# Kernel tuning notes

Measured on AMD Instinct MI355X. Metric: run time of the kernel, lower is better.

## Reference

```python
import jax, jax.numpy as jnp
import numpy as np
import math


def _strided_value_mask(L, S, dtype):
    # mask_line[L + d] == 0 when |d| is a power-of-two stride in {2,4,...,<=L};
    # value_mask[i, j] = mask_line[L - i + j], i.e. zero where |j - i| is such a stride.
    diff = jnp.abs(jnp.arange(L)[:, None] - jnp.arange(S)[None, :])  # [L, S]
    vm = jnp.ones((L, S), dtype=dtype)
    stride = 2
    while stride <= L:
        vm = vm * (diff != stride).astype(dtype)
        stride *= 2
    return vm


def setup_inputs() -> dict:
    key = jax.random.key(0)
    k1, k2, k3 = jax.random.split(key, 3)
    B, L, H, E = 4, 2048, 8, 64
    D = 64
    return {
        "queries": jax.random.normal(k1, (B, L, H, E), dtype=jnp.float32),
        "keys": jax.random.normal(k2, (B, L, H, E), dtype=jnp.float32),
        "values": jax.random.normal(k3, (B, L, H, D), dtype=jnp.float32),
    }


def reference(queries, keys, values):
    B, L, H, E = queries.shape
    S = keys.shape[1]
    scale = 1.0 / math.sqrt(E)

    # raw scores [B, H, L, S]
    scores = jnp.einsum("blhe,bshe->bhls", queries, keys)
    # multiplicative strided mask (zeroes scores at power-of-two offsets)
    vm = _strided_value_mask(L, S, scores.dtype)  # [L, S]
    scores = scores * vm
    # causal mask: upper triangle -> -inf (mask_flag=True, attn_mask=None path)
    causal = jnp.triu(jnp.ones((L, S), dtype=bool), k=1)
    scores = jnp.where(causal, -jnp.inf, scores)

    # dropout p=0.0 (eval) -> identity
    A = jax.nn.softmax(scale * scores, axis=-1)
    V = jnp.einsum("bhls,bshd->blhd", A, values)
    return V
```

## Files before the change

### kernel.cpp

```cpp
#include <hip/hip_runtime.h>
#include <hip/hip_bf16.h>
#include <stdint.h>

typedef __attribute__((ext_vector_type(8))) short short8;
typedef __attribute__((ext_vector_type(16))) float f32x16;

namespace {
constexpr int NB = 4, NL = 2048, NH = 8, NE = 64, ND = 64;
constexpr float KS = 0.125f * 1.44269504f;
constexpr int RECSZ32 = 2080;
constexpr int NUNIT   = 160;
constexpr int NCHUNK = 40;
constexpr int RECSZ  = 8320;
constexpr int KSTEP  = 64 * NH * NE;
}

__device__ const unsigned char ORD[160] = {
  63,127,191,255,
  48,112,176, 49,113,177, 50,114,178, 51,115,179, 52,116,180,
  53,117,181, 54,118,182, 55,119,183, 56,120,184, 57,121,185,
  58,122,186, 59,123,187, 60,124,188, 61,125,189, 62,126,190,
  47,111,175,
  32,96, 33,97, 34,98, 35,99, 36,100, 37,101, 38,102, 39,103,
  40,104, 41,105, 42,106, 43,107, 44,108, 45,109, 46,110,
  31,95,
  15,16,17,18,19,20,21,22,23,24,25,26,27,28,29,30,
  14,94,174,254, 13,93,173,253, 12,92,172,252, 11,91,171,251,
  10,90,170,250,  9,89,169,249,  8,88,168,248,  7,87,167,247,
   6,86,166,246,  5,85,165,245,  4,84,164,244,  3,83,163,243,
   2,82,162,242,  1,81,161,241,  0,80,160,240};

__device__ const unsigned char TG[40] = {
  3,7,7,10,11,11,11,14,14,15,15,15,15,
  6,6,9,9,10,10,12,12,13,13,13,13,14,14,
  2,5,5,8,8,8,9,12,12,
  4,4,1,0};
__device__ const unsigned char TT0[40] = {
  0,0,16,0,0,16,32,0,16,0,16,32,48,
  0,14,0,14,16,30,0,14,0,14,28,42,32,46,
  0,0,12,0,12,24,28,28,40,
  0,10,0,0};
__device__ const unsigned char TT1[40] = {
  16,16,32,16,16,32,48,16,32,16,32,48,64,
  14,28,14,28,30,44,14,28,14,28,42,56,46,60,
  12,12,24,12,24,36,40,40,52,
  10,20,8,4};
__device__ const unsigned char TREC[40] = {
  3,10,11,18,21,22,23,32,33,36,37,38,39,
  8,9,15,16,19,20,24,25,28,29,30,31,34,35,
  2,6,7,12,13,14,17,26,27,
  4,5,1,0};
__device__ const unsigned char CUMD[16] = {0,1,2,3,4,6,8,10,12,15,18,21,24,28,32,36};
__device__ const unsigned char NCHD[16] = {1,1,1,1,2,2,2,2,3,3,3,3,4,4,4,4};

__device__ __forceinline__ ushort bfb(float x) {
  __hip_bfloat16 b(x);
  return __builtin_bit_cast(ushort, b);
}
__device__ __forceinline__ uint32_t pkbf(float lo, float hi) {
  return (uint32_t)bfb(lo) | ((uint32_t)bfb(hi) << 16);
}


__global__ __launch_bounds__(256)
void convfrag(const float* __restrict__ Kg, const float* __restrict__ Vg,
              char* __restrict__ kimg, char* __restrict__ vimg)
{
  const int id = blockIdx.x;
  const int kr = id & 31, bh = id >> 5;
  const int b = bh >> 3, h = bh & 7;
  const int tid = threadIdx.x;

  __shared__ __align__(16) char  kt[64 * 128];
  __shared__ __align__(16) float vt[64 * 64];

  const int key = tid >> 2;
  const int e0  = (tid & 3) * 16;
  {
    const float* kp = Kg + (((size_t)b * NL + kr * 64 + key) * NH + h) * NE + e0;
    float4 a = *(const float4*)kp,       c = *(const float4*)(kp + 4);
    float4 d2 = *(const float4*)(kp + 8), f = *(const float4*)(kp + 12);
    uint4 wA = { pkbf(a.x,a.y), pkbf(a.z,a.w), pkbf(c.x,c.y), pkbf(c.z,c.w) };
    uint4 wB = { pkbf(d2.x,d2.y), pkbf(d2.z,d2.w), pkbf(f.x,f.y), pkbf(f.z,f.w) };
    const int sw = (key & 7) << 4;
    *(uint4*)(kt + key * 128 + ((2 * e0)      ^ sw)) = wA;
    *(uint4*)(kt + key * 128 + ((2 * e0 + 16) ^ sw)) = wB;
  }
  {
    const float* vp = Vg + (((size_t)b * NL + kr * 64 + key) * NH + h) * ND + e0;
    float* dst = vt + key * 64 + e0;
    *(float4*)(dst)      = *(const float4*)(vp);
    *(float4*)(dst + 4)  = *(const float4*)(vp + 4);
    *(float4*)(dst + 8)  = *(const float4*)(vp + 8);
    *(float4*)(dst + 12) = *(const float4*)(vp + 12);
  }
  __syncthreads();

  char* kob = kimg + (size_t)bh * 262144 + (size_t)kr * 2 * 4096;
  char* vob = vimg + (size_t)bh * 262144 + (size_t)kr * 2 * 4096;
  #pragma unroll
  for (int it = 0; it < 2; ++it) {
    int lin = it * 256 + tid;
    int fi = lin >> 6, l = lin & 63;
    int tt = fi >> 2, st = fi & 3;
    int ky = tt * 32 + (l & 31);
    int e  = st * 16 + (l >> 5) * 8;
    uint4 w = *(const uint4*)(kt + ky * 128 + ((2 * e) ^ ((ky & 7) << 4)));
    *(uint4*)(kob + tt * 4096 + st * 1024 + l * 16) = w;
  }
  #pragma unroll
  for (int it = 0; it < 2; ++it) {
    int lin = it * 256 + tid;
    int fi = lin >> 6, l = lin & 63;
    int tt = fi >> 2, f = fi & 3;
    int d  = (f >> 1) * 32 + (l & 31);
    int k0 = tt * 32 + (f & 1) * 16 + (l >> 5) * 8;
    const float* c0 = vt + k0 * 64 + d;
    uint4 w = { pkbf(c0[0],   c0[64]),  pkbf(c0[128], c0[192]),
                pkbf(c0[256], c0[320]), pkbf(c0[384], c0[448]) };
    *(uint4*)(vob + tt * 4096 + f * 1024 + l * 16) = w;
  }
}

__global__ __launch_bounds__(128)
void sattn_frag(const float* __restrict__ Qg, const char* __restrict__ kimg,
                const char* __restrict__ vimg, float* __restrict__ W)
{
  const int id   = blockIdx.x;
  const int bh   = id & 31;
  const int pair = id >> 5;
  const int b = bh >> 3, h = bh & 7;

  const int tid  = threadIdx.x;
  const int wave = tid >> 6;
  const int lane = tid & 63;
  const int ln31 = lane & 31;
  const int hi   = lane >> 5;

  const int e   = ORD[pair * 2 + wave];
  const int s   = e & 63, k = e >> 6;
  const int t0u = k * 16;
  const int t1u = (t0u + 16 < s + 1) ? t0u + 16 : s + 1;
  const int G   = s >> 4;
  const int rix = 8 * G * (G + 1) + (s & 15) * (G + 1) + k;
  float* rec = W + ((size_t)bh * NUNIT + rix) * RECSZ32;

  const int q0w = s * 32;
  const int qi  = q0w + ln31;
  const char* kb_img = kimg + (size_t)bh * 262144 + lane * 16;
  const char* vb_img = vimg + (size_t)bh * 262144 + lane * 16;

  short8 qf[4];
  {
    const float* qp = Qg + (((size_t)b * NL + qi) * NH + h) * NE;
    #pragma unroll
    for (int st = 0; st < 4; ++st) {
      const float* qpe = qp + st * 16 + hi * 8;
      union { short8 v; uint32_t u[4]; } f;
      #pragma unroll
      for (int j = 0; j < 4; ++j)
        f.u[j] = pkbf(qpe[2 * j] * KS, qpe[2 * j + 1] * KS);
      qf[st] = f.v;
    }
  }
  short8 onesv;
  {
    union { short8 v; uint32_t u[4]; } o;
    #pragma unroll
    for (int j = 0; j < 4; ++j) o.u[j] = 0x3F803F80u;
    onesv = o.v;
  }

  f32x16 acc0, acc1, accl;
  #pragma unroll
  for (int i = 0; i < 16; ++i) { acc0[i] = 0.f; acc1[i] = 0.f; accl[i] = 0.f; }

  for (int t = t0u; t < t1u; ++t) {
    const char* kp = kb_img + (size_t)t * 4096;
    const char* vp = vb_img + (size_t)t * 4096;
    short8 a00 = *(const short8*)(vp);
    short8 a01 = *(const short8*)(vp + 1024);
    short8 a10 = *(const short8*)(vp + 2048);
    short8 a11 = *(const short8*)(vp + 3072);
    short8 kf0 = *(const short8*)(kp);
    short8 kf1 = *(const short8*)(kp + 1024);
    short8 kf2 = *(const short8*)(kp + 2048);
    short8 kf3 = *(const short8*)(kp + 3072);

    f32x16 sv;
    #pragma unroll
    for (int i = 0; i < 16; ++i) sv[i] = 0.f;
    sv = __builtin_amdgcn_mfma_f32_32x32x16_bf16(kf0, qf[0], sv, 0, 0, 0);
    sv = __builtin_amdgcn_mfma_f32_32x32x16_bf16(kf1, qf[1], sv, 0, 0, 0);
    sv = __builtin_amdgcn_mfma_f32_32x32x16_bf16(kf2, qf[2], sv, 0, 0, 0);
    sv = __builtin_amdgcn_mfma_f32_32x32x16_bf16(kf3, qf[3], sv, 0, 0, 0);

    const int kv0 = t * 32;
    const int delta = q0w - kv0;
    const int qrelh = (qi - kv0) - 4 * hi;
    if (t == s) {
      #pragma unroll
      for (int r = 0; r < 16; ++r) {
        const int cr = (r & 3) + 8 * (r >> 2);
        int diff = qrelh - cr;
        float lg = sv[r];
        bool p2 = (diff > 1) & ((diff & (diff - 1)) == 0);
        lg = p2 ? 0.f : lg;
        lg = (diff < 0) ? -__builtin_inff() : lg;
        sv[r] = exp2f(lg);
      }
    } else {
      int pmax = 1 << (31 - __clz(delta + 31));
      if (pmax >= delta - 31) {
        #pragma unroll
        for (int r = 0; r < 16; ++r) {
          const int cr = (r & 3) + 8 * (r >> 2);
          int diff = qrelh - cr;
          bool p2 = (diff > 1) & ((diff & (diff - 1)) == 0);
          sv[r] = exp2f(p2 ? 0.f : sv[r]);
        }
      } else {
        #pragma unroll
        for (int r = 0; r < 16; ++r) sv[r] = exp2f(sv[r]);
      }
    }

    uint32_t w0 = pkbf(sv[0],  sv[1]),  w1 = pkbf(sv[2],  sv[3]);
    uint32_t w2 = pkbf(sv[4],  sv[5]),  w3 = pkbf(sv[6],  sv[7]);
    uint32_t w4 = pkbf(sv[8],  sv[9]),  w5 = pkbf(sv[10], sv[11]);
    uint32_t w6 = pkbf(sv[12], sv[13]), w7 = pkbf(sv[14], sv[15]);
    uint32_t y0 = __shfl_xor(hi ? w0 : w2, 32);
    uint32_t y1 = __shfl_xor(hi ? w1 : w3, 32);
    uint32_t y2 = __shfl_xor(hi ? w4 : w6, 32);
    uint32_t y3 = __shfl_xor(hi ? w5 : w7, 32);
    union { short8 v; uint32_t u[4]; } f0, f1;
    if (hi == 0) {
      f0.u[0] = w0; f0.u[1] = w1; f0.u[2] = y0; f0.u[3] = y1;
      f1.u[0] = w4; f1.u[1] = w5; f1.u[2] = y2; f1.u[3] = y3;
    } else {
      f0.u[0] = y0; f0.u[1] = y1; f0.u[2] = w2; f0.u[3] = w3;
      f1.u[0] = y2; f1.u[1] = y3; f1.u[2] = w6; f1.u[3] = w7;
    }

    acc0 = __builtin_amdgcn_mfma_f32_32x32x16_bf16(a00, f0.v, acc0, 0, 0, 0);
    acc0 = __builtin_amdgcn_mfma_f32_32x32x16_bf16(a01, f1.v, acc0, 0, 0, 0);
    acc1 = __builtin_amdgcn_mfma_f32_32x32x16_bf16(a10, f0.v, acc1, 0, 0, 0);
    acc1 = __builtin_amdgcn_mfma_f32_32x32x16_bf16(a11, f1.v, acc1, 0, 0, 0);
    accl = __builtin_amdgcn_mfma_f32_32x32x16_bf16(onesv, f0.v, accl, 0, 0, 0);
    accl = __builtin_amdgcn_mfma_f32_32x32x16_bf16(onesv, f1.v, accl, 0, 0, 0);
  }

  #pragma unroll
  for (int r = 0; r < 16; ++r) {
    int d = (r & 3) + 8 * (r >> 2) + 4 * hi;
    rec[d * 32 + ln31]        = acc0[r];
    rec[(32 + d) * 32 + ln31] = acc1[r];
  }
  if (hi == 0) rec[2048 + ln31] = accl[0];
}

__global__ __launch_bounds__(256)
void sattn_combine32(const float* __restrict__ W, float* __restrict__ Og)
{
  const int id = blockIdx.x;
  const int s  = id & 63, bh = id >> 6;
  const int b = bh >> 3, h = bh & 7;
  const int tid = threadIdx.x;

  const int G = s >> 4, i = s & 15;
  const int cum = 8 * G * (G + 1) + i * (G + 1);
  const int nc  = G + 1;
  const float* rec0 = W + ((size_t)bh * NUNIT + cum) * RECSZ32;

  __shared__ float sd[64][33];
  __shared__ float Lq[32];

  {
    int d = tid >> 2, q4 = (tid & 3) * 8;
    float4 a0 = {0,0,0,0}, a1 = {0,0,0,0};
    for (int c = 0; c < nc; ++c) {
      const float* rp = rec0 + (size_t)c * RECSZ32 + d * 32 + q4;
      float4 v0 = *(const float4*)rp, v1 = *(const float4*)(rp + 4);
      a0.x += v0.x; a0.y += v0.y; a0.z += v0.z; a0.w += v0.w;
      a1.x += v1.x; a1.y += v1.y; a1.z += v1.z; a1.w += v1.w;
    }
    sd[d][q4+0] = a0.x; sd[d][q4+1] = a0.y; sd[d][q4+2] = a0.z; sd[d][q4+3] = a0.w;
    sd[d][q4+4] = a1.x; sd[d][q4+5] = a1.y; sd[d][q4+6] = a1.z; sd[d][q4+7] = a1.w;
  }
  if (tid < 32) {
    float a = 0.f;
    for (int c = 0; c < nc; ++c) a += rec0[(size_t)c * RECSZ32 + 2048 + tid];
    Lq[tid] = 1.0f / a;
  }
  __syncthreads();
  {
    int q = tid >> 3, d8 = (tid & 7) * 8;
    float l = Lq[q];
    float4 o0 = { sd[d8+0][q]*l, sd[d8+1][q]*l, sd[d8+2][q]*l, sd[d8+3][q]*l };
    float4 o1 = { sd[d8+4][q]*l, sd[d8+5][q]*l, sd[d8+6][q]*l, sd[d8+7][q]*l };
    float* op = Og + (((size_t)b * NL + s * 32 + q) * NH + h) * ND + d8;
    *(float4*)op = o0; *(float4*)(op + 4) = o1;
  }
}

#define LD(RR) do {                                                         \
    const float* kp_ = kpp + (size_t)(RR) * KSTEP;                          \
    const float* vp_ = vpp + (size_t)(RR) * KSTEP;                          \
    kx0 = *(const float4*)(kp_);      kx1 = *(const float4*)(kp_ + 4);      \
    kx2 = *(const float4*)(kp_ + 8);  kx3 = *(const float4*)(kp_ + 12);     \
    vx0 = *(const float4*)(vp_);               vx1 = *(const float4*)(vp_ + NH*ND); \
    vx2 = *(const float4*)(vp_ + 2*NH*ND);     vx3 = *(const float4*)(vp_ + 3*NH*ND); \
  } while (0)

#define STG(KB, VB) do {                                                    \
    uint4 kwA = { pkbf(kx0.x,kx0.y), pkbf(kx0.z,kx0.w),                     \
                  pkbf(kx1.x,kx1.y), pkbf(kx1.z,kx1.w) };                   \
    uint4 kwB = { pkbf(kx2.x,kx2.y), pkbf(kx2.z,kx2.w),                     \
                  pkbf(kx3.x,kx3.y), pkbf(kx3.z,kx3.w) };                   \
    *(uint4*)((KB) + krow*128 + ( kcol2        ^ kswz)) = kwA;              \
    *(uint4*)((KB) + krow*128 + ((kcol2 + 16)  ^ kswz)) = kwB;              \
    _Pragma("unroll")                                                       \
    for (int j_ = 0; j_ < 4; ++j_) {                                        \
      int d_ = vd0 + j_;                                                    \
      char* vr_ = (VB) + d_*128;                                            \
      int vs_ = (d_ & 7) << 4;                                              \
      *(uint32_t*)(vr_ + ((vk0*2    ) ^ vs_)) = pkbf(vx0[j_], vx1[j_]);     \
      *(uint32_t*)(vr_ + ((vk0*2 + 4) ^ vs_)) = pkbf(vx2[j_], vx3[j_]);     \
    }                                                                       \
  } while (0)

#define COMPUTE(TT, SUB, KB, VB) do {                                       \
    const int kv0_ = (TT) * 32;                                             \
    f32x16 s;                                                               \
    _Pragma("unroll")                                                       \
    for (int i_ = 0; i_ < 16; ++i_) s[i_] = 0.f;                            \
    { const char* kb_ = (const char*)(KB) + ((SUB)*32 + ln31) * 128;        \
      _Pragma("unroll")                                                     \
      for (int st_ = 0; st_ < 4; ++st_) {                                   \
        short8 kf_ = *(const short8*)(kb_ + ((st_*32 + hi*16) ^ rsw));      \
        s = __builtin_amdgcn_mfma_f32_32x32x16_bf16(kf_, qf[st_], s, 0,0,0);\
      } }                                                                   \
    const int delta_ = q0w - kv0_;                                          \
    const int qrelh_ = (qi - kv0_) - 4 * hi;                                \
    if ((TT) == tw) {                                                       \
      _Pragma("unroll")                                                     \
      for (int r_ = 0; r_ < 16; ++r_) {                                     \
        const int cr_ = (r_ & 3) + 8 * (r_ >> 2);                           \
        int diff_ = qrelh_ - cr_;                                           \
        float lg_ = s[r_];                                                  \
        bool p2_ = (diff_ > 1) & ((diff_ & (diff_ - 1)) == 0);              \
        lg_ = p2_ ? 0.f : lg_;                                              \
        lg_ = (diff_ < 0) ? -__builtin_inff() : lg_;                        \
        s[r_] = exp2f(lg_);                                                 \
      }                                                                     \
    } else {                                                                \
      int pmax_ = 1 << (31 - __clz(delta_ + 31));                           \
      if (pmax_ >= delta_ - 31) {                                           \
        _Pragma("unroll")                                                   \
        for (int r_ = 0; r_ < 16; ++r_) {                                   \
          const int cr_ = (r_ & 3) + 8 * (r_ >> 2);                         \
          int diff_ = qrelh_ - cr_;                                         \
          bool p2_ = (diff_ > 1) & ((diff_ & (diff_ - 1)) == 0);            \
          s[r_] = exp2f(p2_ ? 0.f : s[r_]);                                 \
        }                                                                   \
      } else {                                                              \
        _Pragma("unroll")                                                   \
        for (int r_ = 0; r_ < 16; ++r_) s[r_] = exp2f(s[r_]);               \
      }                                                                     \
    }                                                                       \
    uint32_t w0_ = pkbf(s[0],  s[1]),  w1_ = pkbf(s[2],  s[3]);             \
    uint32_t w2_ = pkbf(s[4],  s[5]),  w3_ = pkbf(s[6],  s[7]);             \
    uint32_t w4_ = pkbf(s[8],  s[9]),  w5_ = pkbf(s[10], s[11]);            \
    uint32_t w6_ = pkbf(s[12], s[13]), w7_ = pkbf(s[14], s[15]);            \
    uint32_t y0_ = __shfl_xor(hi ? w0_ : w2_, 32);                          \
    uint32_t y1_ = __shfl_xor(hi ? w1_ : w3_, 32);                          \
    uint32_t y2_ = __shfl_xor(hi ? w4_ : w6_, 32);                          \
    uint32_t y3_ = __shfl_xor(hi ? w5_ : w7_, 32);                          \
    union { short8 v; uint32_t u[4]; } f0_, f1_;                            \
    if (hi == 0) {                                                          \
      f0_.u[0] = w0_; f0_.u[1] = w1_; f0_.u[2] = y0_; f0_.u[3] = y1_;       \
      f1_.u[0] = w4_; f1_.u[1] = w5_; f1_.u[2] = y2_; f1_.u[3] = y3_;       \
    } else {                                                                \
      f0_.u[0] = y0_; f0_.u[1] = y1_; f0_.u[2] = w2_; f0_.u[3] = w3_;       \
      f1_.u[0] = y2_; f1_.u[1] = y3_; f1_.u[2] = w6_; f1_.u[3] = w7_;       \
    }                                                                       \
    { const char* vr0_ = (const char*)(VB) + ln31 * 128;                    \
      const char* vr1_ = (const char*)(VB) + (32 + ln31) * 128;             \
      short8 a00_ = *(const short8*)(vr0_ + (((SUB)*64      + hi*16) ^ rsw));\
      short8 a01_ = *(const short8*)(vr0_ + (((SUB)*64 + 32 + hi*16) ^ rsw));\
      short8 a10_ = *(const short8*)(vr1_ + (((SUB)*64      + hi*16) ^ rsw));\
      short8 a11_ = *(const short8*)(vr1_ + (((SUB)*64 + 32 + hi*16) ^ rsw));\
      acc0 = __builtin_amdgcn_mfma_f32_32x32x16_bf16(a00_, f0_.v, acc0, 0,0,0); \
      acc0 = __builtin_amdgcn_mfma_f32_32x32x16_bf16(a01_, f1_.v, acc0, 0,0,0); \
      acc1 = __builtin_amdgcn_mfma_f32_32x32x16_bf16(a10_, f0_.v, acc1, 0,0,0); \
      acc1 = __builtin_amdgcn_mfma_f32_32x32x16_bf16(a11_, f1_.v, acc1, 0,0,0); \
      accl = __builtin_amdgcn_mfma_f32_32x32x16_bf16(onesv, f0_.v, accl, 0,0,0);\
      accl = __builtin_amdgcn_mfma_f32_32x32x16_bf16(onesv, f1_.v, accl, 0,0,0);\
    }                                                                       \
  } while (0)

__global__ __launch_bounds__(256, 3)
void sattn_mid(const float* __restrict__ Qg, const float* __restrict__ Kg,
               const float* __restrict__ Vg, float* __restrict__ W)
{
  const int id = blockIdx.x;
  const int bh = id & 31;
  const int e  = id >> 5;
  const int g  = TG[e];
  const int t0 = TT0[e], t1 = TT1[e];
  float* rec = W + (size_t)(bh * NCHUNK + TREC[e]) * RECSZ;
  const int b = bh >> 3, h = bh & 7;

  const int tid  = threadIdx.x;
  const int wave = tid >> 6;
  const int lane = tid & 63;
  const int ln31 = lane & 31;
  const int hi   = lane >> 5;

  __shared__ __align__(16) struct { ushort kt[64 * 64]; ushort vt[64 * 64]; } lds;

  const int q0w = g * 128 + wave * 32;
  const int qi  = q0w + ln31;
  const int tw  = 4 * g + wave;
  const int rsw = (ln31 & 7) << 4;

  short8 qf[4];
  {
    const float* qp = Qg + (((size_t)b * NL + qi) * NH + h) * NE;
    #pragma unroll
    for (int st = 0; st < 4; ++st) {
      const float* qpe = qp + st * 16 + hi * 8;
      union { short8 v; uint32_t u[4]; } f;
      #pragma unroll
      for (int j = 0; j < 4; ++j)
        f.u[j] = pkbf(qpe[2 * j] * KS, qpe[2 * j + 1] * KS);
      qf[st] = f.v;
    }
  }
  short8 onesv;
  {
    union { short8 v; uint32_t u[4]; } o;
    #pragma unroll
    for (int j = 0; j < 4; ++j) o.u[j] = 0x3F803F80u;
    onesv = o.v;
  }

  f32x16 acc0, acc1, accl;
  #pragma unroll
  for (int i = 0; i < 16; ++i) { acc0[i] = 0.f; acc1[i] = 0.f; accl[i] = 0.f; }

  const int krow = tid >> 2,        kcol = (tid & 3) * 16;
  const int vk0  = (tid & 15) * 4,  vd0  = (tid >> 4) * 4;
  const int kbase = t0 * 32;
  const float* kpp = Kg + (((size_t)b * NL + kbase + krow) * NH + h) * NE + kcol;
  const float* vpp = Vg + (((size_t)b * NL + kbase + vk0 ) * NH + h) * ND + vd0;
  const int kswz  = (krow & 7) << 4;
  const int kcol2 = kcol * 2;

  float4 kx0, kx1, kx2, kx3, vx0, vx1, vx2, vx3;

  const int nr = (t1 - t0) >> 1;
  LD(0);
  STG((char*)lds.kt, (char*)lds.vt);
  __syncthreads();
  if (nr > 1) LD(1);
  for (int r = 0;;) {
    const int tt = t0 + 2 * r;
    if (tt     <= tw) COMPUTE(tt,     0, (char*)lds.kt, (char*)lds.vt);
    if (tt + 1 <= tw) COMPUTE(tt + 1, 1, (char*)lds.kt, (char*)lds.vt);
    if (++r == nr) break;
    __syncthreads();
    STG((char*)lds.kt, (char*)lds.vt);
    __syncthreads();
    if (r + 1 < nr) LD(r + 1);
  }

  #pragma unroll
  for (int r = 0; r < 16; ++r) {
    int d = (r & 3) + 8 * (r >> 2) + 4 * hi;
    rec[d * 128 + wave * 32 + ln31]        = acc0[r];
    rec[(32 + d) * 128 + wave * 32 + ln31] = acc1[r];
  }
  if (hi == 0) rec[8192 + wave * 32 + ln31] = accl[0];
}

__global__ __launch_bounds__(256)
void sattn_combine(const float* __restrict__ W, float* __restrict__ Og)
{
  const int id = blockIdx.x;
  const int h2 = id & 1, g = (id >> 1) & 15, bh = id >> 5;
  const int b = bh >> 3, h = bh & 7;
  const int tid = threadIdx.x;

  __shared__ float sd[64][67];
  __shared__ float Lq[64];

  const float* rec0 = W + (size_t)(bh * NCHUNK + CUMD[g]) * RECSZ;
  const int nc = NCHD[g];

  #pragma unroll
  for (int rep = 0; rep < 4; ++rep) {
    int d  = rep * 16 + (tid >> 4);
    int q4 = (tid & 15) * 4;
    float4 a = {0.f, 0.f, 0.f, 0.f};
    for (int c = 0; c < nc; ++c) {
      float4 v = *(const float4*)(rec0 + (size_t)c * RECSZ + d * 128 + h2 * 64 + q4);
      a.x += v.x; a.y += v.y; a.z += v.z; a.w += v.w;
    }
    sd[d][q4 + 0] = a.x; sd[d][q4 + 1] = a.y;
    sd[d][q4 + 2] = a.z; sd[d][q4 + 3] = a.w;
  }
  if (tid < 64) {
    float a = 0.f;
    for (int c = 0; c < nc; ++c) a += rec0[(size_t)c * RECSZ + 8192 + h2 * 64 + tid];
    Lq[tid] = 1.0f / a;
  }
  __syncthreads();
  #pragma unroll
  for (int rep = 0; rep < 4; ++rep) {
    int q  = rep * 16 + (tid >> 4);
    int d4 = (tid & 15) * 4;
    float l = Lq[q];
    float4 o = { sd[d4][q] * l, sd[d4 + 1][q] * l, sd[d4 + 2][q] * l, sd[d4 + 3][q] * l };
    *(float4*)(Og + (((size_t)b * NL + g * 128 + h2 * 64 + q) * NH + h) * ND + d4) = o;
  }
}

extern "C" void kernel_launch(void* const* d_in, const int* in_sizes, int n_in,
                              void* d_out, int out_size, void* d_ws, size_t ws_size,
                              hipStream_t stream) {
  const float* Q = (const float*)d_in[0];
  const float* K = (const float*)d_in[1];
  const float* V = (const float*)d_in[2];
  float* O = (float*)d_out;
  const size_t recbytes = (size_t)32 * NUNIT * RECSZ32 * sizeof(float);
  const size_t imgsz    = (size_t)32 * 64 * 4096;
  const size_t need_full = recbytes + 2 * imgsz;
  const size_t need_mid  = (size_t)32 * NCHUNK * RECSZ * sizeof(float);
  float* W = (float*)d_ws;
  if (ws_size >= need_full) {
    char* kimg = (char*)d_ws + recbytes;
    char* vimg = kimg + imgsz;
    convfrag       <<<dim3(1024), dim3(256), 0, stream>>>(K, V, kimg, vimg);
    sattn_frag     <<<dim3(2560), dim3(128), 0, stream>>>(Q, kimg, vimg, W);
    sattn_combine32<<<dim3(2048), dim3(256), 0, stream>>>(W, O);
  } else {
    sattn_mid      <<<dim3(32 * NCHUNK), dim3(256), 0, stream>>>(Q, K, V, W);
    sattn_combine  <<<dim3(1024), dim3(256), 0, stream>>>(W, O);
  }
}
```

Measured before the change: 66.93 us.

## Balance split-K chunk sizes, reorder work units, use nontemporal partial stores

After: 74.96 us. +12.0%, slower.

```diff
diff --git a/kernel.cpp b/kernel.cpp
--- a/kernel.cpp
+++ b/kernel.cpp
@@ -4,6 +4,7 @@
 
 typedef __attribute__((ext_vector_type(8))) short short8;
 typedef __attribute__((ext_vector_type(16))) float f32x16;
+typedef __attribute__((ext_vector_type(4))) float f32x4;
 
 namespace {
 constexpr int NB = 4, NL = 2048, NH = 8, NE = 64, ND = 64;
@@ -16,19 +17,16 @@
 }
 
 __device__ const unsigned char ORD[160] = {
-  63,127,191,255,
-  48,112,176, 49,113,177, 50,114,178, 51,115,179, 52,116,180,
-  53,117,181, 54,118,182, 55,119,183, 56,120,184, 57,121,185,
-  58,122,186, 59,123,187, 60,124,188, 61,125,189, 62,126,190,
-  47,111,175,
-  32,96, 33,97, 34,98, 35,99, 36,100, 37,101, 38,102, 39,103,
-  40,104, 41,105, 42,106, 43,107, 44,108, 45,109, 46,110,
-  31,95,
-  15,16,17,18,19,20,21,22,23,24,25,26,27,28,29,30,
-  14,94,174,254, 13,93,173,253, 12,92,172,252, 11,91,171,251,
-  10,90,170,250,  9,89,169,249,  8,88,168,248,  7,87,167,247,
-   6,86,166,246,  5,85,165,245,  4,84,164,244,  3,83,163,243,
-   2,82,162,242,  1,81,161,241,  0,80,160,240};
+  63,127, 191,255, 62,126, 190,254, 61,125, 189,253, 60,124, 188,252,
+  59,123, 187,251, 58,122, 186,250, 57,121, 185,249, 56,120, 184,248,
+  55,119, 183,247, 54,118, 182,246, 53,117, 181,245, 52,116, 180,244,
+  51,115, 179,243, 50,114, 178,242, 49,113, 177,241, 48,112, 176,240,
+  47,111, 46,110, 45,109, 44,108, 43,107, 42,106, 41,105, 40,104,
+  39,103, 38,102, 37,101, 36,100, 35,99, 34,98, 33,97, 32,96,
+  175,174, 173,172, 171,170, 169,168, 167,166, 165,164, 163,162, 161,160,
+  31,95, 30,94, 29,93, 28,92, 27,91, 26,90, 25,89, 24,88,
+  23,87, 22,86, 21,85, 20,84, 19,83, 18,82, 17,81, 16,80,
+  15,14, 13,12, 11,10, 9,8, 7,6, 5,4, 3,2, 1,0};
 
 __device__ const unsigned char TG[40] = {
   3,7,7,10,11,11,11,14,14,15,15,15,15,
@@ -60,6 +58,12 @@
 __device__ __forceinline__ uint32_t pkbf(float lo, float hi) {
   return (uint32_t)bfb(lo) | ((uint32_t)bfb(hi) << 16);
 }
+__device__ __forceinline__ void nts(float* p, float v) {
+  __builtin_nontemporal_store(v, p);
+}
+__device__ __forceinline__ f32x4 ntl4(const float* p) {
+  return __builtin_nontemporal_load((const f32x4*)p);
+}
 
 
 __global__ __launch_bounds__(256)
@@ -137,11 +141,12 @@
   const int ln31 = lane & 31;
   const int hi   = lane >> 5;
 
-  const int e   = ORD[pair * 2 + wave];
-  const int s   = e & 63, k = e >> 6;
-  const int t0u = k * 16;
-  const int t1u = (t0u + 16 < s + 1) ? t0u + 16 : s + 1;
-  const int G   = s >> 4;
+  const int e = ORD[pair * 2 + wave];
+  const int s = e & 63, k = e >> 6;
+  const int G = s >> 4, n = G + 1, m = s + 1;
+  const int base = m / n, rem = m % n;
+  const int t0u = k * base + (k < rem ? k : rem);
+  const int t1u = t0u + base + (k < rem ? 1 : 0);
   const int rix = 8 * G * (G + 1) + (s & 15) * (G + 1) + k;
   float* rec = W + ((size_t)bh * NUNIT + rix) * RECSZ32;
 
@@ -253,10 +258,10 @@
   #pragma unroll
   for (int r = 0; r < 16; ++r) {
     int d = (r & 3) + 8 * (r >> 2) + 4 * hi;
-    rec[d * 32 + ln31]        = acc0[r];
-    rec[(32 + d) * 32 + ln31] = acc1[r];
-  }
-  if (hi == 0) rec[2048 + ln31] = accl[0];
+    nts(&rec[d * 32 + ln31],        acc0[r]);
+    nts(&rec[(32 + d) * 32 + ln31], acc1[r]);
+  }
+  if (hi == 0) nts(&rec[2048 + ln31], accl[0]);
 }
 
 __global__ __launch_bounds__(256)
@@ -277,19 +282,19 @@
 
   {
     int d = tid >> 2, q4 = (tid & 3) * 8;
-    float4 a0 = {0,0,0,0}, a1 = {0,0,0,0};
+    f32x4 a0 = {0,0,0,0}, a1 = {0,0,0,0};
     for (int c = 0; c < nc; ++c) {
       const float* rp = rec0 + (size_t)c * RECSZ32 + d * 32 + q4;
-      float4 v0 = *(const float4*)rp, v1 = *(const float4*)(rp + 4);
-      a0.x += v0.x; a0.y += v0.y; a0.z += v0.z; a0.w += v0.w;
-      a1.x += v1.x; a1.y += v1.y; a1.z += v1.z; a1.w += v1.w;
+      f32x4 v0 = ntl4(rp), v1 = ntl4(rp + 4);
+      a0 += v0; a1 += v1;
     }
     sd[d][q4+0] = a0.x; sd[d][q4+1] = a0.y; sd[d][q4+2] = a0.z; sd[d][q4+3] = a0.w;
     sd[d][q4+4] = a1.x; sd[d][q4+5] = a1.y; sd[d][q4+6] = a1.z; sd[d][q4+7] = a1.w;
   }
   if (tid < 32) {
     float a = 0.f;
-    for (int c = 0; c < nc; ++c) a += rec0[(size_t)c * RECSZ32 + 2048 + tid];
+    for (int c = 0; c < nc; ++c)
+      a += __builtin_nontemporal_load(rec0 + (size_t)c * RECSZ32 + 2048 + tid);
     Lq[tid] = 1.0f / a;
   }
   __syncthreads();
```
